# Optimization experiments

Measured on AMD Instinct MI355X. Metric: run time of the kernel, lower is better.

## Reference

```python
import jax, jax.numpy as jnp
import numpy as np

D_MODEL = 1024
NUM_HEADS = 16
THETA = 10000.0
BATCH = 2
SEQ = 2048


def setup_inputs() -> dict:
    key = jax.random.key(0)
    ks = jax.random.split(key, 5)
    std = (2.0 / (D_MODEL + D_MODEL)) ** 0.5
    mk = lambda k: jax.random.truncated_normal(k, -3.0, 3.0, (D_MODEL, D_MODEL), jnp.float32) * std
    return {
        'x': jax.random.normal(ks[0], (BATCH, SEQ, D_MODEL), jnp.float32),
        'Wq': mk(ks[1]),
        'Wk': mk(ks[2]),
        'Wv': mk(ks[3]),
        'Wo': mk(ks[4]),
        'token_positions': jnp.arange(SEQ, dtype=jnp.int32),
    }


def _apply_rope(x, token_positions, theta):
    # x: (B, H, S, d_k)
    d_k = x.shape[-1]
    freq = 1.0 / theta ** (jnp.arange(0, d_k, 2, dtype=jnp.float32) / d_k)  # (d_k//2,)
    freqs = token_positions.astype(jnp.float32)[:, None] * freq[None, :]   # (S, d_k//2)
    cos, sin = jnp.cos(freqs), jnp.sin(freqs)
    x_real = x[..., 0::2]
    x_imag = x[..., 1::2]
    rot_real = x_real * cos - x_imag * sin
    rot_imag = x_real * sin + x_imag * cos
    # interleave back: (..., d_k//2, 2) -> (..., d_k)
    out = jnp.stack([rot_real, rot_imag], axis=-1)
    return out.reshape(x.shape)


def reference(x, Wq, Wk, Wv, Wo, token_positions):
    B, S, D = x.shape
    H = NUM_HEADS
    d_k = D // H

    def split_heads(t):
        return t.reshape(B, S, H, d_k).transpose(0, 2, 1, 3)  # (B, H, S, d_k)

    Q = split_heads(jnp.einsum('bsd,od->bso', x, Wq))
    K = split_heads(jnp.einsum('bsd,od->bso', x, Wk))
    V = split_heads(jnp.einsum('bsd,od->bso', x, Wv))

    Q = _apply_rope(Q, token_positions, THETA)
    K = _apply_rope(K, token_positions, THETA)

    # naive materialized attention with causal mask, faithful to source
    scores = jnp.einsum('bhqd,bhkd->bhqk', Q, K)
    causal = jnp.tril(jnp.ones((S, S), dtype=bool))  # True = attend
    scores = jnp.where(causal[None, None], scores, -jnp.inf)
    scores = scores / jnp.sqrt(jnp.asarray(d_k, scores.dtype))
    probs = jax.nn.softmax(scores, axis=-1)
    attn = jnp.einsum('bhqk,bhkd->bhqd', probs, V)  # (B, H, S, d_v)

    attn = attn.transpose(0, 2, 1, 3).reshape(B, S, D)
    return jnp.einsum('bsd,od->bso', attn, Wo)
```

## Files before the change

### kernel.cpp

```cpp
#include <hip/hip_runtime.h>
#include <hip/hip_bf16.h>
#include <math.h>

#define NUM_HEADS 16
#define DK 64
#define SEQ 2048
#define BATCHN 2
#define DM 1024
#define BS (BATCHN*SEQ)
#define LSCALE 0.18033688011112042f

typedef __bf16 bf16x8 __attribute__((ext_vector_type(8)));
typedef float floatx4 __attribute__((ext_vector_type(4)));
typedef unsigned short ushort;
typedef unsigned int uint;

__device__ __forceinline__ ushort f2bu(float f){
    union { __hip_bfloat16 h; ushort u; } cv; cv.h = __float2bfloat16(f); return cv.u;
}
__device__ __forceinline__ uint packbf(float a, float b){
    return (uint)f2bu(a) | ((uint)f2bu(b) << 16);
}

__global__ __launch_bounds__(256)
void castall(const float* __restrict__ x,  const float* __restrict__ wq,
             const float* __restrict__ wk, const float* __restrict__ wv,
             const float* __restrict__ wo, const int* __restrict__ pos,
             ushort* __restrict__ xb, ushort* __restrict__ wqkb,
             ushort* __restrict__ wvb, ushort* __restrict__ wob,
             float2* __restrict__ tab)
{
    int bid = blockIdx.x;
    if (bid >= 4096) {
        int idx = (bid - 4096)*256 + threadIdx.x;
        int s = idx >> 5, i = idx & 31;
        float invf = expf(-0.28782313662425575f * (float)i);
        float ang = (float)pos[s] * invf;
        float sn, cs; sincosf(ang, &sn, &cs);
        tab[idx] = make_float2(cs, sn);
        return;
    }
    const float* src; ushort* dst; int off;
    if (bid < 2048)      { src = x;  dst = xb;             off = bid; }
    else if (bid < 2560) { src = wq; dst = wqkb;           off = bid - 2048; }
    else if (bid < 3072) { src = wk; dst = wqkb + 1048576; off = bid - 2560; }
    else if (bid < 3584) { src = wv; dst = wvb;            off = bid - 3072; }
    else                 { src = wo; dst = wob;            off = bid - 3584; }
    int i = off*2048 + threadIdx.x*8;
    float4 a = *(const float4*)(src+i);
    float4 b = *(const float4*)(src+i+4);
    uint4 o;
    o.x = packbf(a.x, a.y);
    o.y = packbf(a.z, a.w);
    o.z = packbf(b.x, b.y);
    o.w = packbf(b.z, b.w);
    *(uint4*)(dst+i) = o;
}

__global__ __launch_bounds__(256)
void proj_fused(const ushort* __restrict__ xb, const ushort* __restrict__ Wqkb,
                const ushort* __restrict__ Wvb, ushort* __restrict__ Qb,
                ushort* __restrict__ VTp, const float2* __restrict__ rope)
{
    __shared__ ushort As[128][40];
    __shared__ ushort Bs[128][40];

    const int bid = blockIdx.x;
    const ushort* A; const ushort* W; int row0, col0, mode;
    if (bid < 512) { A = xb;  W = Wqkb; row0 = (bid >> 4) * 128;
                     col0 = (bid & 15) * 128;  mode = 1; }
    else           { int i = bid - 512; A = Wvb; W = xb;
                     row0 = (i >> 5) * 128; col0 = (i & 31) * 128; mode = 2; }

    const int t = threadIdx.x;
    const int w = t >> 6;
    const int L = t & 63;
    const int lr = L & 15;
    const int lq = L >> 4;
    const int wrow = w * 32;

    floatx4 acc[2][8];
    #pragma unroll
    for (int i = 0; i < 2; ++i)
        #pragma unroll
        for (int j = 0; j < 8; ++j)
            acc[i][j] = (floatx4){0.f,0.f,0.f,0.f};

    const int rr = t >> 2, ko = (t & 3) * 8;

    for (int k0 = 0; k0 < DM; k0 += 32) {
        const ushort* ap = A + (size_t)(row0 + rr) * DM + k0 + ko;
        uint4 va  = *(const uint4*)ap;
        uint4 va2 = *(const uint4*)(ap + (size_t)64 * DM);
        const ushort* wp = W + (size_t)(col0 + rr) * DM + k0 + ko;
        uint4 vb  = *(const uint4*)wp;
        uint4 vb2 = *(const uint4*)(wp + (size_t)64 * DM);
        *(uint4*)&As[rr][ko]      = va;
        *(uint4*)&As[rr + 64][ko] = va2;
        *(uint4*)&Bs[rr][ko]      = vb;
        *(uint4*)&Bs[rr + 64][ko] = vb2;
        __syncthreads();

        bf16x8 aF0 = *(const bf16x8*)&As[wrow + lr][lq*8];
        bf16x8 aF1 = *(const bf16x8*)&As[wrow + 16 + lr][lq*8];
        #pragma unroll
        for (int tc = 0; tc < 8; ++tc) {
            bf16x8 bF = *(const bf16x8*)&Bs[tc*16 + lr][lq*8];
            acc[0][tc] = __builtin_amdgcn_mfma_f32_16x16x32_bf16(aF0, bF, acc[0][tc], 0, 0, 0);
            acc[1][tc] = __builtin_amdgcn_mfma_f32_16x16x32_bf16(aF1, bF, acc[1][tc], 0, 0, 0);
        }
        __syncthreads();
    }

    if (mode == 2) {
        #pragma unroll
        for (int tr = 0; tr < 2; ++tr)
            #pragma unroll
            for (int tc = 0; tc < 8; ++tc)
                #pragma unroll
                for (int r = 0; r < 4; ++r) {
                    int m = row0 + wrow + tr*16 + lq*4 + r;
                    int c = col0 + tc*16 + lr;
                    VTp[(size_t)m * BS + c] = f2bu(acc[tr][tc][r]);
                }
    } else {
        const int mat = col0 >> 10;
        const int base_hh = (col0 & 1023) >> 6;
        ushort* out = Qb + (size_t)mat * (BATCHN*NUM_HEADS*SEQ*DK);
        const float qscale = mat ? 1.f : LSCALE;
        #pragma unroll
        for (int tr = 0; tr < 2; ++tr)
            #pragma unroll
            for (int tc = 0; tc < 8; ++tc)
                #pragma unroll
                for (int r = 0; r < 4; ++r) {
                    int m = row0 + wrow + tr*16 + lq*4 + r;
                    int b = m >> 11;
                    int s = m & (SEQ - 1);
                    int dd = (tc*16 + lr) & 63;
                    int hh = base_hh + (tc >> 2);
                    float v = acc[tr][tc][r];
                    float o = __shfl_xor(v, 1, 64);
                    float2 cs = rope[s*32 + (dd >> 1)];
                    float rv = (dd & 1) ? fmaf(o, cs.y,  v * cs.x)
                                        : fmaf(-o, cs.y, v * cs.x);
                    out[((size_t)((b*NUM_HEADS + hh)*SEQ + s))*DK + dd] =
                        f2bu(rv * qscale);
                }
    }
}

__global__ __launch_bounds__(256)
void gemm_out(const ushort* __restrict__ A, const ushort* __restrict__ W,
              float* __restrict__ out)
{
    __shared__ ushort As[128][40];
    __shared__ ushort Bs[128][40];

    const int t = threadIdx.x;
    const int w = t >> 6;
    const int L = t & 63;
    const int lr = L & 15;
    const int lq = L >> 4;
    const int row0 = blockIdx.y * 128;
    const int col0 = blockIdx.x * 128;
    const int wrow = w * 32;

    floatx4 acc[2][8];
    #pragma unroll
    for (int i = 0; i < 2; ++i)
        #pragma unroll
        for (int j = 0; j < 8; ++j)
            acc[i][j] = (floatx4){0.f,0.f,0.f,0.f};

    const int rr = t >> 2, ko = (t & 3) * 8;

    for (int k0 = 0; k0 < DM; k0 += 32) {
        const ushort* ap = A + (size_t)(row0 + rr) * DM + k0 + ko;
        uint4 va  = *(const uint4*)ap;
        uint4 va2 = *(const uint4*)(ap + (size_t)64 * DM);
        const ushort* wp = W + (size_t)(col0 + rr) * DM + k0 + ko;
        uint4 vb  = *(const uint4*)wp;
        uint4 vb2 = *(const uint4*)(wp + (size_t)64 * DM);
        *(uint4*)&As[rr][ko]      = va;
        *(uint4*)&As[rr + 64][ko] = va2;
        *(uint4*)&Bs[rr][ko]      = vb;
        *(uint4*)&Bs[rr + 64][ko] = vb2;
        __syncthreads();

        bf16x8 aF0 = *(const bf16x8*)&As[wrow + lr][lq*8];
        bf16x8 aF1 = *(const bf16x8*)&As[wrow + 16 + lr][lq*8];
        #pragma unroll
        for (int tc = 0; tc < 8; ++tc) {
            bf16x8 bF = *(const bf16x8*)&Bs[tc*16 + lr][lq*8];
            acc[0][tc] = __builtin_amdgcn_mfma_f32_16x16x32_bf16(aF0, bF, acc[0][tc], 0, 0, 0);
            acc[1][tc] = __builtin_amdgcn_mfma_f32_16x16x32_bf16(aF1, bF, acc[1][tc], 0, 0, 0);
        }
        __syncthreads();
    }

    #pragma unroll
    for (int tr = 0; tr < 2; ++tr)
        #pragma unroll
        for (int tc = 0; tc < 8; ++tc)
            #pragma unroll
            for (int r = 0; r < 4; ++r) {
                int m = row0 + wrow + tr*16 + lq*4 + r;
                int c = col0 + tc*16 + lr;
                out[(size_t)m * DM + c] = acc[tr][tc][r];
            }
}

__global__ __launch_bounds__(256)
void attn_mfma(const ushort* __restrict__ Qb, const ushort* __restrict__ Kb,
               const ushort* __restrict__ VT, ushort* __restrict__ attnb,
               float* __restrict__ Opart, float* __restrict__ lpart)
{
    __shared__ ushort Ks[64][72];
    __shared__ ushort Vs[64][72];
    __shared__ ushort Ps[4][16][72];

    const int t = threadIdx.x;
    const int w = t >> 6;
    const int L = t & 63;
    const int lr = L & 15, lq = L >> 4;
    const int h  = blockIdx.y;
    const int b  = blockIdx.z;

    int qt, t0, t1, chunk = 0; bool split;
    {
        const int bx = blockIdx.x;
        if (bx < 16) { qt = bx; t0 = 0; t1 = qt + 1; split = false; }
        else {
            int c2 = bx - 16; qt = 16 + (c2 >> 1); chunk = c2 & 1;
            int nt = qt + 1, half = nt >> 1;
            t0 = chunk ? half : 0; t1 = chunk ? nt : half; split = true;
        }
    }
    const int ntfull = qt + 1;
    const int q0 = qt * 64;
    const int qw = q0 + w * 16;
    const size_t qkbase = (size_t)(b*NUM_HEADS + h) * SEQ * DK;

    bf16x8 qF0, qF1;
    {
        const ushort* qp = Qb + qkbase + (size_t)(qw + lr) * DK + lq*8;
        qF0 = *(const bf16x8*)qp;
        qF1 = *(const bf16x8*)(qp + 32);
    }

    floatx4 O[4];
    #pragma unroll
    for (int g = 0; g < 4; ++g) O[g] = (floatx4){0.f,0.f,0.f,0.f};
    float l_lane = 0.f;

    const int sr = t >> 3, sc = (t & 7) * 8;
    const ushort* kp0 = Kb + qkbase + (size_t)sr * DK + sc;
    const ushort* vp0 = VT + ((size_t)(h*DK + sr)) * BS + b*SEQ + sc;

    for (int tile = t0; tile < t1; ++tile) {
        const int kb = tile * 64;
        __syncthreads();
        {
            uint4 k0v = *(const uint4*)(kp0 + (size_t)kb * DK);
            uint4 k1v = *(const uint4*)(kp0 + (size_t)(kb + 32) * DK);
            uint4 v0v = *(const uint4*)(vp0 + kb);
            uint4 v1v = *(const uint4*)(vp0 + (size_t)32 * BS + kb);
            *(uint4*)&Ks[sr][sc]      = k0v;
            *(uint4*)&Ks[sr + 32][sc] = k1v;
            *(uint4*)&Vs[sr][sc]      = v0v;
            *(uint4*)&Vs[sr + 32][sc] = v1v;
        }
        __syncthreads();

        const bool lastt = (tile == ntfull - 1);
        const int lim = qw + lr - kb;

        #pragma unroll
        for (int g = 0; g < 4; ++g) {
            floatx4 s = (floatx4){0.f,0.f,0.f,0.f};
            bf16x8 kf0 = *(const bf16x8*)&Ks[g*16 + lr][lq*8];
            bf16x8 kf1 = *(const bf16x8*)&Ks[g*16 + lr][32 + lq*8];
            s = __builtin_amdgcn_mfma_f32_16x16x32_bf16(kf0, qF0, s, 0, 0, 0);
            s = __builtin_amdgcn_mfma_f32_16x16x32_bf16(kf1, qF1, s, 0, 0, 0);
            float p0, p1, p2, p3;
            if (lastt) {
                const int kbase = g*16 + lq*4;
                p0 = (kbase + 0 <= lim) ? exp2f(s[0]) : 0.f;
                p1 = (kbase + 1 <= lim) ? exp2f(s[1]) : 0.f;
                p2 = (kbase + 2 <= lim) ? exp2f(s[2]) : 0.f;
                p3 = (kbase + 3 <= lim) ? exp2f(s[3]) : 0.f;
            } else {
                p0 = exp2f(s[0]); p1 = exp2f(s[1]);
                p2 = exp2f(s[2]); p3 = exp2f(s[3]);
            }
            l_lane += (p0 + p1) + (p2 + p3);
            uint2 pk;
            pk.x = packbf(p0, p1);
            pk.y = packbf(p2, p3);
            *(uint2*)&Ps[w][lr][g*16 + lq*4] = pk;
        }
        asm volatile("s_waitcnt lgkmcnt(0)" ::: "memory");

        #pragma unroll
        for (int c = 0; c < 2; ++c) {
            bf16x8 pF = *(const bf16x8*)&Ps[w][lr][c*32 + lq*8];
            #pragma unroll
            for (int g2 = 0; g2 < 4; ++g2) {
                bf16x8 vf = *(const bf16x8*)&Vs[g2*16 + lr][c*32 + lq*8];
                O[g2] = __builtin_amdgcn_mfma_f32_16x16x32_bf16(pF, vf, O[g2], 0, 0, 0);
            }
        }
    }

    l_lane += __shfl_xor(l_lane, 16, 64);
    l_lane += __shfl_xor(l_lane, 32, 64);

    if (!split) {
        #pragma unroll
        for (int r = 0; r < 4; ++r) {
            float lv = __shfl(l_lane, lq*4 + r, 64);
            float li = 1.f / lv;
            int s = qw + lq*4 + r;
            #pragma unroll
            for (int g2 = 0; g2 < 4; ++g2)
                attnb[((size_t)(b*SEQ + s))*DM + h*DK + g2*16 + lr] = f2bu(O[g2][r] * li);
        }
    } else {
        const size_t tb = (size_t)((b*NUM_HEADS + h)*16 + (qt - 16)) * 2 + chunk;
        float* Op = Opart + tb * 4096;
        #pragma unroll
        for (int r = 0; r < 4; ++r) {
            int ql = w*16 + lq*4 + r;
            #pragma unroll
            for (int g2 = 0; g2 < 4; ++g2)
                Op[ql*64 + g2*16 + lr] = O[g2][r];
        }
        if (lq == 0) lpart[tb*64 + w*16 + lr] = l_lane;
    }
}

__global__ __launch_bounds__(256)
void combine(const float* __restrict__ Opart, const float* __restrict__ lpart,
             ushort* __restrict__ attnb)
{
    int gx = blockIdx.x;
    int qti = gx & 15, bh = gx >> 4;
    int h = bh & 15, b = bh >> 4;
    int qt = 16 + qti;
    int tid = threadIdx.x;
    int row = tid >> 2, c0 = (tid & 3) * 16;
    size_t tb = (size_t)(bh*16 + qti) * 2;
    const float* O0 = Opart + tb*4096 + row*64 + c0;
    const float* O1 = O0 + 4096;
    float l = lpart[tb*64 + row] + lpart[tb*64 + 64 + row];
    float li = 1.f / l;
    int s = qt*64 + row;
    ushort* dst = attnb + ((size_t)(b*SEQ + s))*DM + h*DK + c0;
    #pragma unroll
    for (int e = 0; e < 16; e += 4) {
        float4 a = *(const float4*)(O0 + e);
        float4 c = *(const float4*)(O1 + e);
        dst[e+0] = f2bu((a.x + c.x) * li);
        dst[e+1] = f2bu((a.y + c.y) * li);
        dst[e+2] = f2bu((a.z + c.z) * li);
        dst[e+3] = f2bu((a.w + c.w) * li);
    }
}

extern "C" void kernel_launch(void* const* d_in, const int* in_sizes, int n_in,
                              void* d_out, int out_size, void* d_ws, size_t ws_size,
                              hipStream_t stream) {
    const float* x   = (const float*)d_in[0];
    const float* Wq  = (const float*)d_in[1];
    const float* Wk  = (const float*)d_in[2];
    const float* Wv  = (const float*)d_in[3];
    const float* Wo  = (const float*)d_in[4];
    const int*   pos = (const int*)d_in[5];
    float* out = (float*)d_out;

    const size_t MB = 1u << 20;
    char* ws = (char*)d_ws;
    ushort* xb    = (ushort*)(ws);
    ushort* Wqkb  = (ushort*)(ws +  8*MB);
    ushort* Wvb   = (ushort*)(ws + 12*MB);
    float*  Opart = (float*)(ws);
    float*  lpart = (float*)(ws + 17*MB);
    ushort* Qb    = (ushort*)(ws + 18*MB);
    ushort* Kb    = (ushort*)(ws + 26*MB);
    ushort* VT    = (ushort*)(ws + 34*MB);
    ushort* attnb = (ushort*)(ws + 42*MB);
    float2* ropeT = (float2*)(ws + 50*MB);
    ushort* Wob   = (ushort*)(ws + 51*MB);

    dim3 blk(256);
    castall<<<4352, blk, 0, stream>>>(x, Wq, Wk, Wv, Wo, pos,
                                      xb, Wqkb, Wvb, Wob, ropeT);

    proj_fused<<<768, blk, 0, stream>>>(xb, Wqkb, Wvb, Qb, VT, ropeT);

    attn_mfma<<<dim3(48, NUM_HEADS, BATCHN), blk, 0, stream>>>(Qb, Kb, VT, attnb,
                                                               Opart, lpart);
    combine<<<512, blk, 0, stream>>>(Opart, lpart, attnb);

    gemm_out<<<dim3(8,32), blk, 0, stream>>>(attnb, Wob, out);
}
```

Baseline: 224.0 us.

## Use direct global-to-LDS loads, finer attention split-K, bf16 partials, smaller out tiles

After: 200.8 us. -10.4%, faster.

```diff
diff --git a/kernel.cpp b/kernel.cpp
--- a/kernel.cpp
+++ b/kernel.cpp
@@ -20,6 +20,14 @@
 }
 __device__ __forceinline__ uint packbf(float a, float b){
     return (uint)f2bu(a) | ((uint)f2bu(b) << 16);
+}
+__device__ __forceinline__ float bu2f(ushort u){
+    union { uint u; float f; } cv; cv.u = (uint)u << 16; return cv.f;
+}
+__device__ __forceinline__ void gl16(const void* g, void* l){
+    __builtin_amdgcn_global_load_lds(
+        (const __attribute__((address_space(1))) unsigned int*)g,
+        (__attribute__((address_space(3))) unsigned int*)l, 16, 0, 0);
 }
 
 __global__ __launch_bounds__(256)
@@ -62,8 +70,8 @@
                 const ushort* __restrict__ Wvb, ushort* __restrict__ Qb,
                 ushort* __restrict__ VTp, const float2* __restrict__ rope)
 {
-    __shared__ ushort As[128][40];
-    __shared__ ushort Bs[128][40];
+    __shared__ ushort As[128][32];
+    __shared__ ushort Bs[128][32];
 
     const int bid = blockIdx.x;
     const ushort* A; const ushort* W; int row0, col0, mode;
@@ -87,18 +95,15 @@
             acc[i][j] = (floatx4){0.f,0.f,0.f,0.f};
 
     const int rr = t >> 2, ko = (t & 3) * 8;
+    const ushort* ga = A + (size_t)(row0 + rr) * DM + ko;
+    const ushort* gb = W + (size_t)(col0 + rr) * DM + ko;
 
     for (int k0 = 0; k0 < DM; k0 += 32) {
-        const ushort* ap = A + (size_t)(row0 + rr) * DM + k0 + ko;
-        uint4 va  = *(const uint4*)ap;
-        uint4 va2 = *(const uint4*)(ap + (size_t)64 * DM);
-        const ushort* wp = W + (size_t)(col0 + rr) * DM + k0 + ko;
-        uint4 vb  = *(const uint4*)wp;
-        uint4 vb2 = *(const uint4*)(wp + (size_t)64 * DM);
-        *(uint4*)&As[rr][ko]      = va;
-        *(uint4*)&As[rr + 64][ko] = va2;
-        *(uint4*)&Bs[rr][ko]      = vb;
-        *(uint4*)&Bs[rr + 64][ko] = vb2;
+        __syncthreads();
+        gl16(ga + k0,                    &As[rr][ko]);
+        gl16(ga + k0 + (size_t)64*DM,    &As[rr + 64][ko]);
+        gl16(gb + k0,                    &Bs[rr][ko]);
+        gl16(gb + k0 + (size_t)64*DM,    &Bs[rr + 64][ko]);
         __syncthreads();
 
         bf16x8 aF0 = *(const bf16x8*)&As[wrow + lr][lq*8];
@@ -109,7 +114,6 @@
             acc[0][tc] = __builtin_amdgcn_mfma_f32_16x16x32_bf16(aF0, bF, acc[0][tc], 0, 0, 0);
             acc[1][tc] = __builtin_amdgcn_mfma_f32_16x16x32_bf16(aF1, bF, acc[1][tc], 0, 0, 0);
         }
-        __syncthreads();
     }
 
     if (mode == 2) {
@@ -154,8 +158,8 @@
 void gemm_out(const ushort* __restrict__ A, const ushort* __restrict__ W,
               float* __restrict__ out)
 {
-    __shared__ ushort As[128][40];
-    __shared__ ushort Bs[128][40];
+    __shared__ ushort As[128][32];
+    __shared__ ushort Bs[64][32];
 
     const int t = threadIdx.x;
     const int w = t >> 6;
@@ -163,46 +167,41 @@
     const int lr = L & 15;
     const int lq = L >> 4;
     const int row0 = blockIdx.y * 128;
-    const int col0 = blockIdx.x * 128;
+    const int col0 = blockIdx.x * 64;
     const int wrow = w * 32;
 
-    floatx4 acc[2][8];
+    floatx4 acc[2][4];
     #pragma unroll
     for (int i = 0; i < 2; ++i)
         #pragma unroll
-        for (int j = 0; j < 8; ++j)
+        for (int j = 0; j < 4; ++j)
             acc[i][j] = (floatx4){0.f,0.f,0.f,0.f};
 
     const int rr = t >> 2, ko = (t & 3) * 8;
+    const ushort* ga = A + (size_t)(row0 + rr) * DM + ko;
+    const ushort* gb = W + (size_t)(col0 + rr) * DM + ko;
 
     for (int k0 = 0; k0 < DM; k0 += 32) {
-        const ushort* ap = A + (size_t)(row0 + rr) * DM + k0 + ko;
-        uint4 va  = *(const uint4*)ap;
-        uint4 va2 = *(const uint4*)(ap + (size_t)64 * DM);
-        const ushort* wp = W + (size_t)(col0 + rr) * DM + k0 + ko;
-        uint4 vb  = *(const uint4*)wp;
-        uint4 vb2 = *(const uint4*)(wp + (size_t)64 * DM);
-        *(uint4*)&As[rr][ko]      = va;
-        *(uint4*)&As[rr + 64][ko] = va2;
-        *(uint4*)&Bs[rr][ko]      = vb;
-        *(uint4*)&Bs[rr + 64][ko] = vb2;
+        __syncthreads();
+        gl16(ga + k0,                 &As[rr][ko]);
+        gl16(ga + k0 + (size_t)64*DM, &As[rr + 64][ko]);
+        gl16(gb + k0,                 &Bs[rr][ko]);
         __syncthreads();
 
         bf16x8 aF0 = *(const bf16x8*)&As[wrow + lr][lq*8];
         bf16x8 aF1 = *(const bf16x8*)&As[wrow + 16 + lr][lq*8];
         #pragma unroll
-        for (int tc = 0; tc < 8; ++tc) {
+        for (int tc = 0; tc < 4; ++tc) {
             bf16x8 bF = *(const bf16x8*)&Bs[tc*16 + lr][lq*8];
             acc[0][tc] = __builtin_amdgcn_mfma_f32_16x16x32_bf16(aF0, bF, acc[0][tc], 0, 0, 0);
             acc[1][tc] = __builtin_amdgcn_mfma_f32_16x16x32_bf16(aF1, bF, acc[1][tc], 0, 0, 0);
         }
-        __syncthreads();
     }
 
     #pragma unroll
     for (int tr = 0; tr < 2; ++tr)
         #pragma unroll
-        for (int tc = 0; tc < 8; ++tc)
+        for (int tc = 0; tc < 4; ++tc)
             #pragma unroll
             for (int r = 0; r < 4; ++r) {
                 int m = row0 + wrow + tr*16 + lq*4 + r;
@@ -214,7 +213,7 @@
 __global__ __launch_bounds__(256)
 void attn_mfma(const ushort* __restrict__ Qb, const ushort* __restrict__ Kb,
                const ushort* __restrict__ VT, ushort* __restrict__ attnb,
-               float* __restrict__ Opart, float* __restrict__ lpart)
+               ushort* __restrict__ Opart, float* __restrict__ lpart)
 {
     __shared__ ushort Ks[64][72];
     __shared__ ushort Vs[64][72];
@@ -227,17 +226,17 @@
     const int h  = blockIdx.y;
     const int b  = blockIdx.z;
 
-    int qt, t0, t1, chunk = 0; bool split;
+    int qt, chunk, nch;
     {
         const int bx = blockIdx.x;
-        if (bx < 16) { qt = bx; t0 = 0; t1 = qt + 1; split = false; }
-        else {
-            int c2 = bx - 16; qt = 16 + (c2 >> 1); chunk = c2 & 1;
-            int nt = qt + 1, half = nt >> 1;
-            t0 = chunk ? half : 0; t1 = chunk ? nt : half; split = true;
-        }
-    }
-    const int ntfull = qt + 1;
+        if (bx < 8)       { qt = bx;              chunk = 0;     nch = 1; }
+        else if (bx < 24) { int i = bx - 8;  qt = 8  + (i>>1); chunk = i&1;        nch = 2; }
+        else if (bx < 48) { int i = bx - 24; int q3 = i/3; qt = 16 + q3; chunk = i - q3*3; nch = 3; }
+        else              { int i = bx - 48; qt = 24 + (i>>2); chunk = i&3;        nch = 4; }
+    }
+    const int nt = qt + 1;
+    const int t0 = (nt * chunk) / nch;
+    const int t1 = (nt * (chunk + 1)) / nch;
     const int q0 = qt * 64;
     const int qw = q0 + w * 16;
     const size_t qkbase = (size_t)(b*NUM_HEADS + h) * SEQ * DK;
@@ -273,7 +272,7 @@
         }
         __syncthreads();
 
-        const bool lastt = (tile == ntfull - 1);
+        const bool lastt = (tile == nt - 1);
         const int lim = qw + lr - kb;
 
         #pragma unroll
@@ -316,7 +315,7 @@
     l_lane += __shfl_xor(l_lane, 16, 64);
     l_lane += __shfl_xor(l_lane, 32, 64);
 
-    if (!split) {
+    if (nch == 1) {
         #pragma unroll
         for (int r = 0; r < 4; ++r) {
             float lv = __shfl(l_lane, lq*4 + r, 64);
@@ -327,45 +326,54 @@
                 attnb[((size_t)(b*SEQ + s))*DM + h*DK + g2*16 + lr] = f2bu(O[g2][r] * li);
         }
     } else {
-        const size_t tb = (size_t)((b*NUM_HEADS + h)*16 + (qt - 16)) * 2 + chunk;
-        float* Op = Opart + tb * 4096;
+        const int slot = ((b*NUM_HEADS + h)*24 + (qt - 8))*4 + chunk;
+        ushort* Op = Opart + (size_t)slot * 4096;
         #pragma unroll
         for (int r = 0; r < 4; ++r) {
             int ql = w*16 + lq*4 + r;
             #pragma unroll
             for (int g2 = 0; g2 < 4; ++g2)
-                Op[ql*64 + g2*16 + lr] = O[g2][r];
-        }
-        if (lq == 0) lpart[tb*64 + w*16 + lr] = l_lane;
+                Op[ql*64 + g2*16 + lr] = f2bu(O[g2][r]);
+        }
+        if (lq == 0) lpart[(size_t)slot*64 + w*16 + lr] = l_lane;
     }
 }
 
 __global__ __launch_bounds__(256)
-void combine(const float* __restrict__ Opart, const float* __restrict__ lpart,
+void combine(const ushort* __restrict__ Opart, const float* __restrict__ lpart,
              ushort* __restrict__ attnb)
 {
     int gx = blockIdx.x;
-    int qti = gx & 15, bh = gx >> 4;
+    int qti = gx % 24, bh = gx / 24;
     int h = bh & 15, b = bh >> 4;
-    int qt = 16 + qti;
+    int qt = 8 + qti;
+    int nch = (qt >> 3) + 1;
     int tid = threadIdx.x;
     int row = tid >> 2, c0 = (tid & 3) * 16;
-    size_t tb = (size_t)(bh*16 + qti) * 2;
-    const float* O0 = Opart + tb*4096 + row*64 + c0;
-    const float* O1 = O0 + 4096;
-    float l = lpart[tb*64 + row] + lpart[tb*64 + 64 + row];
+    const int base_slot = (bh*24 + qti)*4;
+
+    float acc[16];
+    #pragma unroll
+    for (int e = 0; e < 16; ++e) acc[e] = 0.f;
+    float l = 0.f;
+
+    for (int c = 0; c < nch; ++c) {
+        const ushort* Op = Opart + (size_t)(base_slot + c)*4096 + row*64 + c0;
+        uint4 u0 = *(const uint4*)(Op);
+        uint4 u1 = *(const uint4*)(Op + 8);
+        const ushort* h0 = (const ushort*)&u0;
+        const ushort* h1 = (const ushort*)&u1;
+        #pragma unroll
+        for (int e = 0; e < 8; ++e) { acc[e]   += bu2f(h0[e]); }
+        #pragma unroll
+        for (int e = 0; e < 8; ++e) { acc[8+e] += bu2f(h1[e]); }
+        l += lpart[(size_t)(base_slot + c)*64 + row];
+    }
     float li = 1.f / l;
     int s = qt*64 + row;
     ushort* dst = attnb + ((size_t)(b*SEQ + s))*DM + h*DK + c0;
     #pragma unroll
-    for (int e = 0; e < 16; e += 4) {
-        float4 a = *(const float4*)(O0 + e);
-        float4 c = *(const float4*)(O1 + e);
-        dst[e+0] = f2bu((a.x + c.x) * li);
-        dst[e+1] = f2bu((a.y + c.y) * li);
-        dst[e+2] = f2bu((a.z + c.z) * li);
-        dst[e+3] = f2bu((a.w + c.w) * li);
-    }
+    for (int e = 0; e < 16; ++e) dst[e] = f2bu(acc[e] * li);
 }
 
 extern "C" void kernel_launch(void* const* d_in, const int* in_sizes, int n_in,
@@ -384,14 +392,14 @@
     ushort* xb    = (ushort*)(ws);
     ushort* Wqkb  = (ushort*)(ws +  8*MB);
     ushort* Wvb   = (ushort*)(ws + 12*MB);
-    float*  Opart = (float*)(ws);
-    float*  lpart = (float*)(ws + 17*MB);
-    ushort* Qb    = (ushort*)(ws + 18*MB);
-    ushort* Kb    = (ushort*)(ws + 26*MB);
-    ushort* VT    = (ushort*)(ws + 34*MB);
-    ushort* attnb = (ushort*)(ws + 42*MB);
-    float2* ropeT = (float2*)(ws + 50*MB);
-    ushort* Wob   = (ushort*)(ws + 51*MB);
+    ushort* Opart = (ushort*)(ws);
+    float*  lpart = (float*)(ws + 24*MB);
+    ushort* Qb    = (ushort*)(ws + 25*MB);
+    ushort* Kb    = (ushort*)(ws + 33*MB);
+    ushort* VT    = (ushort*)(ws + 41*MB);
+    ushort* attnb = (ushort*)(ws + 49*MB);
+    float2* ropeT = (float2*)(ws + 57*MB);
+    ushort* Wob   = (ushort*)(ws + 58*MB);
 
     dim3 blk(256);
     castall<<<4352, blk, 0, stream>>>(x, Wq, Wk, Wv, Wo, pos,
@@ -399,9 +407,9 @@
 
     proj_fused<<<768, blk, 0, stream>>>(xb, Wqkb, Wvb, Qb, VT, ropeT);
 
-    attn_mfma<<<dim3(48, NUM_HEADS, BATCHN), blk, 0, stream>>>(Qb, Kb, VT, attnb,
+    attn_mfma<<<dim3(80, NUM_HEADS, BATCHN), blk, 0, stream>>>(Qb, Kb, VT, attnb,
                                                                Opart, lpart);
-    combine<<<512, blk, 0, stream>>>(Opart, lpart, attnb);
-
-    gemm_out<<<dim3(8,32), blk, 0, stream>>>(attnb, Wob, out);
-}
+    combine<<<768, blk, 0, stream>>>(Opart, lpart, attnb);
+
+    gemm_out<<<dim3(16,32), blk, 0, stream>>>(attnb, Wob, out);
+}
```
